# Optimization experiments

Measured on AMD Instinct MI355X. Metric: run time of the kernel, lower is better.

The kernel has to match this reference:

```python
import jax, jax.numpy as jnp
import numpy as np

N_NODES = 100000
N_EDGES = 1600000
EMB = 128


def setup_inputs() -> dict:
    key = jax.random.key(0)
    k1, k2, k3, k4, k5, k6 = jax.random.split(key, 6)
    embeddings = jax.random.normal(k1, (N_NODES, EMB), dtype=jnp.float32)
    edge_row = jax.random.randint(k2, (N_EDGES,), 0, N_NODES, dtype=jnp.int32)
    edge_col = jax.random.randint(k3, (N_EDGES,), 0, N_NODES, dtype=jnp.int32)
    edge_val = jax.random.uniform(k4, (N_EDGES,), dtype=jnp.float32)
    W1 = jax.random.normal(k5, (EMB, EMB), dtype=jnp.float32) * (1.0 / np.sqrt(EMB))
    W2 = jax.random.normal(k6, (EMB, EMB), dtype=jnp.float32) * (1.0 / np.sqrt(EMB))
    return {"embeddings": embeddings, "edge_row": edge_row, "edge_col": edge_col,
            "edge_val": edge_val, "W1": W1, "W2": W2}


def reference(embeddings, edge_row, edge_col, edge_val, W1, W2):
    # SpMM: relevant = A @ embeddings, A in COO form (row, col, val), shape [N, N]
    gathered = embeddings[edge_col] * edge_val[:, None]          # [E, D]
    relevant = jax.ops.segment_sum(gathered, edge_row, num_segments=N_NODES)  # [N, D]
    # non-interactive + interactive messages
    non_interactive = relevant @ W1                               # [N, D]
    interactive = (relevant * embeddings) @ W2                    # [N, D]
    return non_interactive + interactive
```

## Files before the change

kernel.cpp:

```cpp
#include <hip/hip_runtime.h>
#include <hip/hip_bf16.h>
#include <stdint.h>

#define NN 100000
#define NE 1600000
#define DD 128
#define NBLK 98
#define NBKT 16
#define RPB 6250
#define NCHK 16
#define PBLK 512
#define PTHR 256
#define PCHUNK 3125
#define SEGCAP 288

typedef __attribute__((ext_vector_type(8))) short short8;
typedef __attribute__((ext_vector_type(4))) float f32x4;

__device__ inline unsigned bf16bits(float x) {
  __hip_bfloat16 h = __float2bfloat16(x);
  return (unsigned)*reinterpret_cast<unsigned short*>(&h);
}

__device__ inline float bfhi(unsigned u) { return __uint_as_float(u & 0xffff0000u); }
__device__ inline float bflo(unsigned u) { return __uint_as_float(u << 16); }

__global__ __launch_bounds__(256) void k_prep(
    const float* __restrict__ emb, uint4* __restrict__ tbl,
    const float* __restrict__ W1, const float* __restrict__ W2,
    uint4* __restrict__ wpack) {
  int gid = blockIdx.x * 256 + threadIdx.x;
  if (blockIdx.x < 6250) {
    const float4 a = ((const float4*)emb)[2 * gid];
    const float4 b = ((const float4*)emb)[2 * gid + 1];
    uint4 u;
    u.x = bf16bits(a.x) | (bf16bits(a.y) << 16);
    u.y = bf16bits(a.z) | (bf16bits(a.w) << 16);
    u.z = bf16bits(b.x) | (bf16bits(b.y) << 16);
    u.w = bf16bits(b.z) | (bf16bits(b.w) << 16);
    tbl[gid] = u;
  } else {
    int cid = (blockIdx.x - 6250) * 256 + threadIdx.x;
    int lane = cid & 63, ct = (cid >> 6) & 7, ks = cid >> 9;
    int colc = ct * 16 + (lane & 15);
    int k0 = ks * 32 + (lane >> 4) * 8;
    unsigned h[8];
#pragma unroll
    for (int j = 0; j < 8; ++j) {
      int kk = k0 + j;
      float w = (kk < DD) ? W1[kk * DD + colc] : W2[(kk - DD) * DD + colc];
      h[j] = bf16bits(w);
    }
    uint4 u;
    u.x = h[0] | (h[1] << 16);
    u.y = h[2] | (h[3] << 16);
    u.z = h[4] | (h[5] << 16);
    u.w = h[6] | (h[7] << 16);
    wpack[cid] = u;
  }
}

__global__ __launch_bounds__(256) void k_bscatter3(
    const int* __restrict__ row, const int* __restrict__ col,
    const float* __restrict__ val, uint2* __restrict__ ebuf,
    int* __restrict__ bcnt) {
  __shared__ int lcnt[NBKT];
  const int t = threadIdx.x;
  if (t < NBKT) lcnt[t] = 0;
  __syncthreads();
  const int e0 = blockIdx.x * PCHUNK;
  const size_t segbase = (size_t)blockIdx.x * NBKT * SEGCAP;
#pragma unroll 2
  for (int base = 0; base < PCHUNK; base += PTHR) {
    int off = base + t;
    if (off < PCHUNK) {
      int i = e0 + off;
      int r = row[i];
      int m = r / RPB;
      uint2 e;
      e.x = ((unsigned)col[i] << 15) | (bf16bits(val[i]) & 0x7fffu);
      e.y = (unsigned)r;
      int idx = atomicAdd(&lcnt[m], 1);
      if (idx < SEGCAP) ebuf[segbase + (size_t)m * SEGCAP + idx] = e;
    }
  }
  __syncthreads();
  if (t < NBKT) bcnt[blockIdx.x * NBKT + t] = min(lcnt[t], SEGCAP);
}

__global__ __launch_bounds__(1024) void k_hist(const uint2* __restrict__ ebuf,
                                               const int* __restrict__ bcnt,
                                               int* __restrict__ partial) {
  __shared__ int h[RPB];
  const int m = blockIdx.x & 15, c = blockIdx.x >> 4;
  for (int i = threadIdx.x; i < RPB; i += 1024) h[i] = 0;
  __syncthreads();
  const int base = m * RPB;
  for (int b = c * 32; b < c * 32 + 32; ++b) {
    int scnt = bcnt[b * NBKT + m];
    const uint2* src = ebuf + ((size_t)b * NBKT + m) * SEGCAP;
    for (int i = threadIdx.x; i < scnt; i += 1024)
      atomicAdd(&h[(int)src[i].y - base], 1);
  }
  __syncthreads();
  int* dst = partial + (m * NCHK + c) * RPB;
  for (int i = threadIdx.x; i < RPB; i += 1024) dst[i] = h[i];
}

__global__ __launch_bounds__(1024) void k_scan1(int* __restrict__ partial,
                                                int* __restrict__ offsets,
                                                int* __restrict__ bsum) {
  __shared__ int wsum[16];
  const int t = threadIdx.x, lane = t & 63, wid = t >> 6;
  int i = blockIdx.x * 1024 + t;
  int v = 0;
  if (i < NN) {
    int m = i / RPB, rl = i - m * RPB;
    int* p = partial + (m * NCHK) * RPB + rl;
    int s = 0;
#pragma unroll
    for (int cc = 0; cc < NCHK; ++cc) {
      int x = p[cc * RPB];
      p[cc * RPB] = s;
      s += x;
    }
    v = s;
  }
  int incl = v;
#pragma unroll
  for (int d = 1; d < 64; d <<= 1) {
    int u = __shfl_up(incl, d, 64);
    if (lane >= d) incl += u;
  }
  if (lane == 63) wsum[wid] = incl;
  __syncthreads();
  if (wid == 0) {
    int w = (lane < 16) ? wsum[lane] : 0;
#pragma unroll
    for (int d = 1; d < 16; d <<= 1) {
      int u = __shfl_up(w, d, 64);
      if (lane >= d) w += u;
    }
    if (lane < 16) wsum[lane] = w;
  }
  __syncthreads();
  int wbase = wid ? wsum[wid - 1] : 0;
  if (i < NN) offsets[i] = wbase + incl - v;
  if (t == 0) bsum[blockIdx.x] = wsum[15];
}

__global__ void k_scan2(const int* __restrict__ bsum, int* __restrict__ bpre) {
  const int lane = threadIdx.x;
  int a = bsum[lane];
  int b = (lane + 64 < NBLK) ? bsum[lane + 64] : 0;
  int sa = a, sb = b;
#pragma unroll
  for (int d = 1; d < 64; d <<= 1) {
    int u = __shfl_up(sa, d, 64);
    if (lane >= d) sa += u;
    u = __shfl_up(sb, d, 64);
    if (lane >= d) sb += u;
  }
  int totA = __shfl(sa, 63, 64);
  bpre[lane] = sa - a;
  if (lane + 64 < NBLK) bpre[lane + 64] = totA + sb - b;
}

__global__ __launch_bounds__(1024) void k_scatter3(
    const uint2* __restrict__ ebuf, const int* __restrict__ bcnt,
    const int* __restrict__ partial, const int* __restrict__ offsets,
    const int* __restrict__ bpre, unsigned* __restrict__ cpack) {
  __shared__ int cur[RPB];
  const int m = blockIdx.x & 15, c = blockIdx.x >> 4;
  const int base = m * RPB;
  const int* pre = partial + (m * NCHK + c) * RPB;
  for (int i = threadIdx.x; i < RPB; i += 1024) {
    int r = base + i;
    cur[i] = offsets[r] + bpre[r >> 10] + pre[i];
  }
  __syncthreads();
  for (int b = c * 32; b < c * 32 + 32; ++b) {
    int scnt = bcnt[b * NBKT + m];
    const uint2* src = ebuf + ((size_t)b * NBKT + m) * SEGCAP;
    for (int i = threadIdx.x; i < scnt; i += 1024) {
      uint2 e = src[i];
      int pos = atomicAdd(&cur[(int)e.y - base], 1);
      cpack[pos] = e.x;
    }
  }
}

__global__ __launch_bounds__(256) void k_spmm(
    const int* __restrict__ offsets, const int* __restrict__ bpre,
    const unsigned* __restrict__ cpack, const unsigned short* __restrict__ tbl,
    unsigned* __restrict__ rel) {
  const int lane = threadIdx.x & 63;
  const int node = blockIdx.x * 4 + (threadIdx.x >> 6);
  if (node >= NN) return;
  const int beg = offsets[node] + bpre[node >> 10];
  const int end = (node + 1 == NN) ? NE : offsets[node + 1] + bpre[(node + 1) >> 10];
  const int half = lane >> 5;
  const int sub = lane & 31;
  float a0 = 0.f, a1 = 0.f, a2 = 0.f, a3 = 0.f;
  for (int j0 = beg; j0 < end; j0 += 64) {
    int idx = j0 + lane;
    unsigned pk = (idx < end) ? cpack[idx] : 0u;
    int n8 = (min(end - j0, 64) + 7) & ~7;
    for (int t = 0; t < n8; t += 8) {
#pragma unroll
      for (int s = 0; s < 4; ++s) {
        unsigned u = (unsigned)__shfl((int)pk, t + 2 * s + half, 64);
        unsigned c = u >> 15;
        float v = __uint_as_float((u << 16) & 0x7fff0000u);
        const uint2 w = *(const uint2*)(tbl + ((size_t)c << 7) + (sub << 2));
        a0 = fmaf(v, bflo(w.x), a0);
        a1 = fmaf(v, bfhi(w.x), a1);
        a2 = fmaf(v, bflo(w.y), a2);
        a3 = fmaf(v, bfhi(w.y), a3);
      }
    }
  }
  a0 += __shfl_xor(a0, 32, 64);
  a1 += __shfl_xor(a1, 32, 64);
  a2 += __shfl_xor(a2, 32, 64);
  a3 += __shfl_xor(a3, 32, 64);
  if (lane < 32) {
    uint2 o;
    o.x = bf16bits(a0) | (bf16bits(a1) << 16);
    o.y = bf16bits(a2) | (bf16bits(a3) << 16);
    *(uint2*)(rel + (size_t)node * 64 + (sub << 1)) = o;
  }
}

__device__ inline short8 bfmul8(short8 a, short8 b) {
  short8 r;
#pragma unroll
  for (int i = 0; i < 8; ++i) {
    float fa = __uint_as_float(((unsigned)(unsigned short)a[i]) << 16);
    float fb = __uint_as_float(((unsigned)(unsigned short)b[i]) << 16);
    r[i] = (short)bf16bits(fa * fb);
  }
  return r;
}

__global__ __launch_bounds__(256) void k_phase2(
    const unsigned short* __restrict__ rel, const unsigned short* __restrict__ tbl,
    const uint4* __restrict__ wpack, float* __restrict__ out) {
  __shared__ uint4 bw[4096];
  for (int i = threadIdx.x; i < 4096; i += 256) bw[i] = wpack[i];
  __syncthreads();

  const int lane = threadIdx.x & 63;
  const int wid = threadIdx.x >> 6;
  const long Rw = (long)blockIdx.x * 128 + wid * 32;

  long r0 = Rw + (lane & 15);
  long r1 = r0 + 16;
  if (r0 >= NN) r0 = NN - 1;
  if (r1 >= NN) r1 = NN - 1;
  const int fo = (lane >> 4) * 8;

  f32x4 acc[2][8] = {};

#pragma unroll
  for (int ks = 0; ks < 4; ++ks) {
    short8 rf0 = *(const short8*)(rel + r0 * DD + ks * 32 + fo);
    short8 ef0 = *(const short8*)(tbl + r0 * DD + ks * 32 + fo);
    short8 rf1 = *(const short8*)(rel + r1 * DD + ks * 32 + fo);
    short8 ef1 = *(const short8*)(tbl + r1 * DD + ks * 32 + fo);
    short8 m0 = bfmul8(rf0, ef0);
    short8 m1 = bfmul8(rf1, ef1);
#pragma unroll
    for (int ct = 0; ct < 8; ++ct) {
      short8 b1 = *(const short8*)&bw[(ks * 8 + ct) * 64 + lane];
      short8 b2 = *(const short8*)&bw[((ks + 4) * 8 + ct) * 64 + lane];
      acc[0][ct] = __builtin_amdgcn_mfma_f32_16x16x32_bf16(rf0, b1, acc[0][ct], 0, 0, 0);
      acc[0][ct] = __builtin_amdgcn_mfma_f32_16x16x32_bf16(m0, b2, acc[0][ct], 0, 0, 0);
      acc[1][ct] = __builtin_amdgcn_mfma_f32_16x16x32_bf16(rf1, b1, acc[1][ct], 0, 0, 0);
      acc[1][ct] = __builtin_amdgcn_mfma_f32_16x16x32_bf16(m1, b2, acc[1][ct], 0, 0, 0);
    }
  }

  const int orow = (lane >> 4) * 4;
  const int ocol = lane & 15;
#pragma unroll
  for (int rt = 0; rt < 2; ++rt) {
    long rbase = Rw + rt * 16 + orow;
#pragma unroll
    for (int ct = 0; ct < 8; ++ct) {
#pragma unroll
      for (int q = 0; q < 4; ++q) {
        long rr = rbase + q;
        if (rr < NN) out[rr * DD + ct * 16 + ocol] = acc[rt][ct][q];
      }
    }
  }
}

extern "C" void kernel_launch(void* const* d_in, const int* in_sizes, int n_in,
                              void* d_out, int out_size, void* d_ws, size_t ws_size,
                              hipStream_t stream) {
  const float* emb = (const float*)d_in[0];
  const int* erow = (const int*)d_in[1];
  const int* ecol = (const int*)d_in[2];
  const float* eva = (const float*)d_in[3];
  const float* W1 = (const float*)d_in[4];
  const float* W2 = (const float*)d_in[5];
  float* out = (float*)d_out;

  char* ws = (char*)d_ws;
  unsigned short* tbl = (unsigned short*)(ws);
  unsigned short* rel = (unsigned short*)(ws + 25600000);
  uint2* ebuf = (uint2*)(ws + 25600000);
  int* partial = (int*)(ws + 25600000 + 18874368);
  int* bcnt = (int*)(ws + 25600000 + 25274368);
  int* offsets = (int*)(ws + 51200000);
  unsigned* cpack = (unsigned*)(ws + 52000128);
  int* bsum = (int*)(ws + 58400128);
  int* bpre = (int*)(ws + 58400640);
  uint4* wpack = (uint4*)(ws + 58401152);

  k_prep<<<6266, 256, 0, stream>>>(emb, (uint4*)tbl, W1, W2, wpack);
  k_bscatter3<<<PBLK, PTHR, 0, stream>>>(erow, ecol, eva, ebuf, bcnt);
  k_hist<<<NBKT * NCHK, 1024, 0, stream>>>(ebuf, bcnt, partial);
  k_scan1<<<NBLK, 1024, 0, stream>>>(partial, offsets, bsum);
  k_scan2<<<1, 64, 0, stream>>>(bsum, bpre);
  k_scatter3<<<NBKT * NCHK, 1024, 0, stream>>>(ebuf, bcnt, partial, offsets, bpre, cpack);
  k_spmm<<<NN / 4, 256, 0, stream>>>(offsets, bpre, cpack, tbl, (unsigned*)rel);
  k_phase2<<<(NN + 127) / 128, 256, 0, stream>>>(rel, tbl, wpack, out);
}
```

Before: 147.0 us.

## Fuse prep with edge bucketing and widen SpMM gathers with software prefetch

Merges the embedding/weight bf16 conversion kernel with the edge bucket-scatter kernel into one launch, so the two independent jobs share a grid and one launch is saved. The SpMM kernel now has each lane gather 16 bytes (8 bf16) instead of 8, so four edges are processed per wave step instead of two. It also double-buffers the next pair of gathered rows before consuming the current pair. The cost is twice as many accumulators per lane and an extra shuffle-reduction stage, which adds register pressure.

```diff
diff --git a/kernel.cpp b/kernel.cpp
--- a/kernel.cpp
+++ b/kernel.cpp
@@ -13,6 +13,7 @@
 #define PTHR 256
 #define PCHUNK 3125
 #define SEGCAP 288
+#define PREPBLK 6266
 
 typedef __attribute__((ext_vector_type(8))) short short8;
 typedef __attribute__((ext_vector_type(4))) float f32x4;
@@ -25,12 +26,37 @@
 __device__ inline float bfhi(unsigned u) { return __uint_as_float(u & 0xffff0000u); }
 __device__ inline float bflo(unsigned u) { return __uint_as_float(u << 16); }
 
-__global__ __launch_bounds__(256) void k_prep(
-    const float* __restrict__ emb, uint4* __restrict__ tbl,
-    const float* __restrict__ W1, const float* __restrict__ W2,
-    uint4* __restrict__ wpack) {
-  int gid = blockIdx.x * 256 + threadIdx.x;
-  if (blockIdx.x < 6250) {
+__global__ __launch_bounds__(256) void k_front(
+    const int* __restrict__ row, const int* __restrict__ col,
+    const float* __restrict__ val, uint2* __restrict__ ebuf,
+    int* __restrict__ bcnt, const float* __restrict__ emb,
+    uint4* __restrict__ tbl, const float* __restrict__ W1,
+    const float* __restrict__ W2, uint4* __restrict__ wpack) {
+  const int t = threadIdx.x;
+  if (blockIdx.x < PBLK) {
+    __shared__ int lcnt[NBKT];
+    if (t < NBKT) lcnt[t] = 0;
+    __syncthreads();
+    const int e0 = blockIdx.x * PCHUNK;
+    const size_t segbase = (size_t)blockIdx.x * NBKT * SEGCAP;
+#pragma unroll 2
+    for (int base = 0; base < PCHUNK; base += PTHR) {
+      int off = base + t;
+      if (off < PCHUNK) {
+        int i = e0 + off;
+        int r = row[i];
+        int m = r / RPB;
+        uint2 e;
+        e.x = ((unsigned)col[i] << 15) | (bf16bits(val[i]) & 0x7fffu);
+        e.y = (unsigned)r;
+        int idx = atomicAdd(&lcnt[m], 1);
+        if (idx < SEGCAP) ebuf[segbase + (size_t)m * SEGCAP + idx] = e;
+      }
+    }
+    __syncthreads();
+    if (t < NBKT) bcnt[blockIdx.x * NBKT + t] = min(lcnt[t], SEGCAP);
+  } else if (blockIdx.x < PBLK + 6250) {
+    int gid = (blockIdx.x - PBLK) * 256 + t;
     const float4 a = ((const float4*)emb)[2 * gid];
     const float4 b = ((const float4*)emb)[2 * gid + 1];
     uint4 u;
@@ -40,7 +66,7 @@
     u.w = bf16bits(b.z) | (bf16bits(b.w) << 16);
     tbl[gid] = u;
   } else {
-    int cid = (blockIdx.x - 6250) * 256 + threadIdx.x;
+    int cid = (blockIdx.x - PBLK - 6250) * 256 + t;
     int lane = cid & 63, ct = (cid >> 6) & 7, ks = cid >> 9;
     int colc = ct * 16 + (lane & 15);
     int k0 = ks * 32 + (lane >> 4) * 8;
@@ -58,34 +84,6 @@
     u.w = h[6] | (h[7] << 16);
     wpack[cid] = u;
   }
-}
-
-__global__ __launch_bounds__(256) void k_bscatter3(
-    const int* __restrict__ row, const int* __restrict__ col,
-    const float* __restrict__ val, uint2* __restrict__ ebuf,
-    int* __restrict__ bcnt) {
-  __shared__ int lcnt[NBKT];
-  const int t = threadIdx.x;
-  if (t < NBKT) lcnt[t] = 0;
-  __syncthreads();
-  const int e0 = blockIdx.x * PCHUNK;
-  const size_t segbase = (size_t)blockIdx.x * NBKT * SEGCAP;
-#pragma unroll 2
-  for (int base = 0; base < PCHUNK; base += PTHR) {
-    int off = base + t;
-    if (off < PCHUNK) {
-      int i = e0 + off;
-      int r = row[i];
-      int m = r / RPB;
-      uint2 e;
-      e.x = ((unsigned)col[i] << 15) | (bf16bits(val[i]) & 0x7fffu);
-      e.y = (unsigned)r;
-      int idx = atomicAdd(&lcnt[m], 1);
-      if (idx < SEGCAP) ebuf[segbase + (size_t)m * SEGCAP + idx] = e;
-    }
-  }
-  __syncthreads();
-  if (t < NBKT) bcnt[blockIdx.x * NBKT + t] = min(lcnt[t], SEGCAP);
 }
 
 __global__ __launch_bounds__(1024) void k_hist(const uint2* __restrict__ ebuf,
@@ -190,45 +188,68 @@
   }
 }
 
+#define CONSUME(U, W)                                          \
+  {                                                            \
+    float v = __uint_as_float(((U) << 16) & 0x7fff0000u);      \
+    a0 = fmaf(v, bflo((W).x), a0);                             \
+    a1 = fmaf(v, bfhi((W).x), a1);                             \
+    a2 = fmaf(v, bflo((W).y), a2);                             \
+    a3 = fmaf(v, bfhi((W).y), a3);                             \
+    a4 = fmaf(v, bflo((W).z), a4);                             \
+    a5 = fmaf(v, bfhi((W).z), a5);                             \
+    a6 = fmaf(v, bflo((W).w), a6);                             \
+    a7 = fmaf(v, bfhi((W).w), a7);                             \
+  }
+
 __global__ __launch_bounds__(256) void k_spmm(
     const int* __restrict__ offsets, const int* __restrict__ bpre,
     const unsigned* __restrict__ cpack, const unsigned short* __restrict__ tbl,
-    unsigned* __restrict__ rel) {
+    uint4* __restrict__ rel) {
   const int lane = threadIdx.x & 63;
   const int node = blockIdx.x * 4 + (threadIdx.x >> 6);
   if (node >= NN) return;
   const int beg = offsets[node] + bpre[node >> 10];
   const int end = (node + 1 == NN) ? NE : offsets[node + 1] + bpre[(node + 1) >> 10];
-  const int half = lane >> 5;
-  const int sub = lane & 31;
+  const int q = lane >> 4;
+  const int sub = lane & 15;
+  const unsigned short* tsub = tbl + (sub << 3);
   float a0 = 0.f, a1 = 0.f, a2 = 0.f, a3 = 0.f;
+  float a4 = 0.f, a5 = 0.f, a6 = 0.f, a7 = 0.f;
   for (int j0 = beg; j0 < end; j0 += 64) {
     int idx = j0 + lane;
     unsigned pk = (idx < end) ? cpack[idx] : 0u;
     int n8 = (min(end - j0, 64) + 7) & ~7;
-    for (int t = 0; t < n8; t += 8) {
-#pragma unroll
-      for (int s = 0; s < 4; ++s) {
-        unsigned u = (unsigned)__shfl((int)pk, t + 2 * s + half, 64);
-        unsigned c = u >> 15;
-        float v = __uint_as_float((u << 16) & 0x7fff0000u);
-        const uint2 w = *(const uint2*)(tbl + ((size_t)c << 7) + (sub << 2));
-        a0 = fmaf(v, bflo(w.x), a0);
-        a1 = fmaf(v, bfhi(w.x), a1);
-        a2 = fmaf(v, bflo(w.y), a2);
-        a3 = fmaf(v, bfhi(w.y), a3);
-      }
-    }
-  }
-  a0 += __shfl_xor(a0, 32, 64);
-  a1 += __shfl_xor(a1, 32, 64);
-  a2 += __shfl_xor(a2, 32, 64);
-  a3 += __shfl_xor(a3, 32, 64);
-  if (lane < 32) {
-    uint2 o;
+    unsigned uA0 = (unsigned)__shfl((int)pk, q, 64);
+    unsigned uA1 = (unsigned)__shfl((int)pk, 4 + q, 64);
+    uint4 wA0 = *(const uint4*)(tsub + ((size_t)(uA0 >> 15) << 7));
+    uint4 wA1 = *(const uint4*)(tsub + ((size_t)(uA1 >> 15) << 7));
+    for (int t = 8; t < n8; t += 8) {
+      unsigned uB0 = (unsigned)__shfl((int)pk, t + q, 64);
+      unsigned uB1 = (unsigned)__shfl((int)pk, t + 4 + q, 64);
+      uint4 wB0 = *(const uint4*)(tsub + ((size_t)(uB0 >> 15) << 7));
+      uint4 wB1 = *(const uint4*)(tsub + ((size_t)(uB1 >> 15) << 7));
+      CONSUME(uA0, wA0);
+      CONSUME(uA1, wA1);
+      uA0 = uB0; wA0 = wB0; uA1 = uB1; wA1 = wB1;
+    }
+    CONSUME(uA0, wA0);
+    CONSUME(uA1, wA1);
+  }
+  a0 += __shfl_xor(a0, 16, 64); a1 += __shfl_xor(a1, 16, 64);
+  a2 += __shfl_xor(a2, 16, 64); a3 += __shfl_xor(a3, 16, 64);
+  a4 += __shfl_xor(a4, 16, 64); a5 += __shfl_xor(a5, 16, 64);
+  a6 += __shfl_xor(a6, 16, 64); a7 += __shfl_xor(a7, 16, 64);
+  a0 += __shfl_xor(a0, 32, 64); a1 += __shfl_xor(a1, 32, 64);
+  a2 += __shfl_xor(a2, 32, 64); a3 += __shfl_xor(a3, 32, 64);
+  a4 += __shfl_xor(a4, 32, 64); a5 += __shfl_xor(a5, 32, 64);
+  a6 += __shfl_xor(a6, 32, 64); a7 += __shfl_xor(a7, 32, 64);
+  if (lane < 16) {
+    uint4 o;
     o.x = bf16bits(a0) | (bf16bits(a1) << 16);
     o.y = bf16bits(a2) | (bf16bits(a3) << 16);
-    *(uint2*)(rel + (size_t)node * 64 + (sub << 1)) = o;
+    o.z = bf16bits(a4) | (bf16bits(a5) << 16);
+    o.w = bf16bits(a6) | (bf16bits(a7) << 16);
+    rel[(size_t)node * 16 + sub] = o;
   }
 }
 
@@ -289,9 +310,9 @@
 #pragma unroll
     for (int ct = 0; ct < 8; ++ct) {
 #pragma unroll
-      for (int q = 0; q < 4; ++q) {
-        long rr = rbase + q;
-        if (rr < NN) out[rr * DD + ct * 16 + ocol] = acc[rt][ct][q];
+      for (int qq = 0; qq < 4; ++qq) {
+        long rr = rbase + qq;
+        if (rr < NN) out[rr * DD + ct * 16 + ocol] = acc[rt][ct][qq];
       }
     }
   }
@@ -320,12 +341,12 @@
   int* bpre = (int*)(ws + 58400640);
   uint4* wpack = (uint4*)(ws + 58401152);
 
-  k_prep<<<6266, 256, 0, stream>>>(emb, (uint4*)tbl, W1, W2, wpack);
-  k_bscatter3<<<PBLK, PTHR, 0, stream>>>(erow, ecol, eva, ebuf, bcnt);
+  k_front<<<PBLK + PREPBLK, 256, 0, stream>>>(erow, ecol, eva, ebuf, bcnt,
+                                              emb, (uint4*)tbl, W1, W2, wpack);
   k_hist<<<NBKT * NCHK, 1024, 0, stream>>>(ebuf, bcnt, partial);
   k_scan1<<<NBLK, 1024, 0, stream>>>(partial, offsets, bsum);
   k_scan2<<<1, 64, 0, stream>>>(bsum, bpre);
   k_scatter3<<<NBKT * NCHK, 1024, 0, stream>>>(ebuf, bcnt, partial, offsets, bpre, cpack);
-  k_spmm<<<NN / 4, 256, 0, stream>>>(offsets, bpre, cpack, tbl, (unsigned*)rel);
+  k_spmm<<<NN / 4, 256, 0, stream>>>(offsets, bpre, cpack, tbl, (uint4*)rel);
   k_phase2<<<(NN + 127) / 128, 256, 0, stream>>>(rel, tbl, wpack, out);
 }
```

Measured after the change: 142.5 us. -3.1%, faster.
